# Performance work log

Measured on AMD Instinct MI355X. Metric: run time of the kernel, lower is better.

The kernel has to match this reference:

```python
import jax, jax.numpy as jnp
import numpy as np

N_SIGMA = 2
FG_W = 1.0
W_INST, W_VAR, W_SEED = 1.0, 10.0, 1.0
N_IDS = 15  # instance ids 1..15 (0 = background)


def _xym(H, W, dtype):
    # torch buffer: xm varies along width, ym along height, linspace over 512 then sliced
    xm = jnp.broadcast_to(jnp.linspace(0.0, 1.0, 512)[:W][None, :], (H, W))
    ym = jnp.broadcast_to(jnp.linspace(0.0, 1.0, 512)[:H][:, None], (H, W))
    return jnp.stack([xm, ym], 0).astype(dtype)  # [2,H,W]


def _lovasz_hinge_flat(logits, gt):
    # canonical Lovasz hinge over a flat image; gt in {0,1} float
    signs = 2.0 * gt - 1.0
    errors = 1.0 - logits * signs
    order = jnp.argsort(-errors)
    errors_sorted = errors[order]
    gt_sorted = gt[order]
    gts = gt_sorted.sum()
    inter = gts - jnp.cumsum(gt_sorted)
    union = gts + jnp.cumsum(1.0 - gt_sorted)
    jacc = 1.0 - inter / union
    grad = jnp.concatenate([jacc[:1], jacc[1:] - jacc[:-1]])
    return jnp.dot(jax.nn.relu(errors_sorted), jax.lax.stop_gradient(grad))


def _loss(prediction, instances, labels):
    B, C, H, W = prediction.shape
    xym = _xym(H, W, prediction.dtype)
    spatial_emb = jnp.tanh(prediction[:, 0:2]) + xym           # [B,2,H,W]
    sigma = prediction[:, 2:2 + N_SIGMA]                       # [B,2,H,W]
    seed = jax.nn.sigmoid(prediction[:, 2 + N_SIGMA])          # [B,H,W]

    ids = jnp.arange(1, N_IDS + 1)
    maskf = (instances[:, None] == ids[None, :, None, None]).astype(prediction.dtype)  # [B,N,H,W]
    counts = maskf.sum((-2, -1))                               # [B,N]
    valid = counts > 0
    safe = jnp.maximum(counts, 1.0)

    centers = jnp.einsum('bchw,bnhw->bnc', spatial_emb, maskf) / safe[..., None]  # [B,N,2]
    s_mean = jnp.einsum('bchw,bnhw->bnc', sigma, maskf) / safe[..., None]         # [B,N,2]
    s_sg = jax.lax.stop_gradient(s_mean)

    # sum over mask of (sigma - s_sg)^2, expanded to avoid a [B,N,2,H,W] tensor
    e2 = jnp.einsum('bchw,bnhw->bnc', sigma * sigma, maskf)
    var_sum = e2 - 2.0 * s_sg * (s_mean * safe[..., None]) + s_sg * s_sg * counts[..., None]
    var_i = var_sum.sum(-1) / (N_SIGMA * safe)                 # torch.mean over [n_sigma, M]

    s_exp = jnp.exp(10.0 * s_mean)                             # [B,N,2] (grad flows, as in torch)
    dist_arg = jnp.zeros((B, N_IDS, H, W), prediction.dtype)
    for c in range(N_SIGMA):  # tiny fixed loop over 2 coordinate channels
        d = spatial_emb[:, c][:, None] - centers[:, :, c][..., None, None]
        dist_arg = dist_arg + s_exp[:, :, c][..., None, None] * d * d
    dist = jnp.exp(-dist_arg)                                  # [B,N,H,W]

    logits = (dist * 2.0 - 1.0).reshape(B * N_IDS, H * W)
    labs = maskf.reshape(B * N_IDS, H * W)
    inst_i = jax.vmap(_lovasz_hinge_flat)(logits, labs).reshape(B, N_IDS)

    seed_i = FG_W * jnp.einsum('bnhw,bnhw->bn', maskf,
                               (seed[:, None] - jax.lax.stop_gradient(dist)) ** 2)

    bg = (labels == 0).astype(prediction.dtype)
    seed_bg = jnp.einsum('bhw,bhw->b', bg, seed * seed)        # (seed - 0)^2 on background

    vf = valid.astype(prediction.dtype)
    obj = jnp.maximum(vf.sum(1), 1.0)
    inst_b = (vf * inst_i).sum(1) / obj
    var_b = (vf * var_i).sum(1) / obj
    seed_b = (seed_bg + (vf * seed_i).sum(1)) / (H * W)
    return jnp.mean(W_INST * inst_b + W_VAR * var_b + W_SEED * seed_b)


def setup_inputs() -> dict:
    key = jax.random.key(0)
    k1, k2, k3 = jax.random.split(key, 3)
    prediction = jax.random.normal(k1, (16, 5, 512, 512), dtype=jnp.float32)
    instances = jax.random.randint(k2, (16, 512, 512), 0, 16, dtype=jnp.int64)
    labels = jax.random.randint(k3, (16, 512, 512), 0, 2, dtype=jnp.int64)
    return {"prediction": prediction, "instances": instances, "labels": labels}


def reference(prediction, instances, labels):
    return _loss(prediction, instances, labels)
```

## Files before the change

kernel.cpp:

```cpp
#include <hip/hip_runtime.h>
#include <hip/hip_fp16.h>
#include <cmath>

#define BATCH 16
#define NID   15
#define NSEG  240
#define HW    262144
#define HEADB 65536
#define NSPL  8
#define NCHK  4
#define PREBLK 512
#define PSTRIDE 112

#define KFINEBASE 30208
#define KOVF 119
#define KTOT 2424

typedef float v2f __attribute__((ext_vector_type(2)));

__device__ __forceinline__ int keyof(float d) {
  unsigned b = __float_as_uint(d);
  return (b >= 0x3B800000u) ? (int)((b >> 15) - KFINEBASE + KOVF) : (int)(b >> 23);
}
__device__ __forceinline__ void boundsof(int k, float* lo, float* hi) {
  if (k >= KOVF) {
    unsigned u = (unsigned)(k - KOVF + KFINEBASE) << 15;
    *lo = __uint_as_float(u);
    *hi = __uint_as_float(u + 32768u);
  } else {
    *lo = __uint_as_float((unsigned)k << 23);
    *hi = __uint_as_float((unsigned)(k + 1) << 23);
  }
}

__device__ __forceinline__ float fast_tanh(float x) {
  float e = __expf(2.0f * x);
  return 1.0f - 2.0f / (e + 1.0f);
}
__device__ __forceinline__ float fast_sigmoid(float x) {
  return 1.0f / (1.0f + __expf(-x));
}

struct Params { float cx, cy, e0, e1, var, valid, cnt; };
__device__ __forceinline__ Params calc_params(const float* __restrict__ st) {
  Params p;
  float cnt = st[0];
  float safe = fmaxf(cnt, 1.0f);
  p.cx = st[1] / safe;
  p.cy = st[2] / safe;
  float m0 = st[3] / safe, m1 = st[4] / safe;
  float v0 = st[5] - 2.0f * m0 * (m0 * safe) + m0 * m0 * cnt;
  float v1 = st[6] - 2.0f * m1 * (m1 * safe) + m1 * m1 * cnt;
  p.var = (v0 + v1) / (2.0f * safe);
  p.e0 = expf(10.0f * m0);
  p.e1 = expf(10.0f * m1);
  p.valid = (cnt > 0.f) ? 1.f : 0.f;
  p.cnt = cnt;
  return p;
}

__global__ void __launch_bounds__(256, 2)
pre_kernel(const float* __restrict__ pred, const int* __restrict__ inst,
           const int* __restrict__ lab, float* __restrict__ blockpart,
           unsigned* __restrict__ exyh, unsigned* __restrict__ tb8,
           unsigned* __restrict__ sd8) {
  __shared__ float ws[4][NID * 7 + 1];
  int tid = threadIdx.x;
  int w = tid >> 6, lane = tid & 63;
  int gid = blockIdx.x;
  int b = gid >> 5, c = gid & 31;
  const float* pb = pred + (size_t)b * 5 * HW;
  const int4* ip = (const int4*)(inst + (size_t)b * HW);
  const int4* lp = (const int4*)(lab + (size_t)b * HW);
  size_t bq = (size_t)b * (HW / 4);
  v2f acc[NID][4];
#pragma unroll
  for (int id = 0; id < NID; ++id)
#pragma unroll
    for (int s = 0; s < 4; ++s) acc[id][s] = (v2f)(0.f);
  float bgacc = 0.f;
  int g0 = c * 2048 + tid;
  float4 A0 = ((const float4*)pb)[g0];
  float4 A1 = ((const float4*)(pb + HW))[g0];
  float4 A2 = ((const float4*)(pb + 2 * HW))[g0];
  float4 A3 = ((const float4*)(pb + 3 * HW))[g0];
  float4 A4 = ((const float4*)(pb + 4 * HW))[g0];
  int4 T4 = ip[g0];
  int4 L4 = lp[g0];
#pragma unroll 1
  for (int it = 0; it < 8; ++it) {
    int g = c * 2048 + it * 256 + tid;
    float4 v0 = A0, v1 = A1, v2 = A2, v3 = A3, v4 = A4;
    int4 t4 = T4, l4 = L4;
    if (it < 7) {
      int gn = g + 256;
      A0 = ((const float4*)pb)[gn];
      A1 = ((const float4*)(pb + HW))[gn];
      A2 = ((const float4*)(pb + 2 * HW))[gn];
      A3 = ((const float4*)(pb + 3 * HW))[gn];
      A4 = ((const float4*)(pb + 4 * HW))[gn];
      T4 = ip[gn];
      L4 = lp[gn];
    }
    float p0a[4] = {v0.x, v0.y, v0.z, v0.w};
    float p1a[4] = {v1.x, v1.y, v1.z, v1.w};
    float p2a[4] = {v2.x, v2.y, v2.z, v2.w};
    float p3a[4] = {v3.x, v3.y, v3.z, v3.w};
    float p4a[4] = {v4.x, v4.y, v4.z, v4.w};
    int ta[4] = {t4.x, t4.y, t4.z, t4.w};
    int la[4] = {l4.x, l4.y, l4.z, l4.w};
    unsigned eo[4], tpack = 0, spack = 0;
    int px0 = g * 4;
#pragma unroll
    for (int k = 0; k < 4; ++k) {
      int px = px0 + k;
      float xm = (float)(px & 511) * (1.0f / 511.0f);
      float ym = (float)(px >> 9) * (1.0f / 511.0f);
      float ex = fast_tanh(p0a[k]) + xm;
      float ey = fast_tanh(p1a[k]) + ym;
      float sd = fast_sigmoid(p4a[k]);
      __half2 h = __floats2half2_rn(ex, ey);
      eo[k] = *reinterpret_cast<unsigned*>(&h);
      int t = ta[k];
      tpack |= ((unsigned)(t & 255)) << (8 * k);
      unsigned sq = (unsigned)(sd * 255.0f + 0.5f);
      spack |= (sq & 255u) << (8 * k);
      float p2 = p2a[k], p3 = p3a[k];
      v2f P01; P01.x = 1.0f; P01.y = ex;
      v2f P23; P23.x = ey;   P23.y = p2;
      v2f P45; P45.x = p3;   P45.y = p2 * p2;
      v2f P67; P67.x = p3 * p3; P67.y = 0.f;
#pragma unroll
      for (int id = 0; id < NID; ++id) {
        float pr = (t == id + 1) ? 1.0f : 0.0f;
        v2f prv; prv.x = pr; prv.y = pr;
        acc[id][0] = prv * P01 + acc[id][0];
        acc[id][1] = prv * P23 + acc[id][1];
        acc[id][2] = prv * P45 + acc[id][2];
        acc[id][3] = prv * P67 + acc[id][3];
      }
      if (la[k] == 0) bgacc += sd * sd;
    }
    ((uint4*)exyh)[bq + g] = make_uint4(eo[0], eo[1], eo[2], eo[3]);
    tb8[bq + g] = tpack;
    sd8[bq + g] = spack;
  }
#pragma unroll
  for (int id = 0; id < NID; ++id) {
    float vals7[7] = {acc[id][0].x, acc[id][0].y, acc[id][1].x, acc[id][1].y,
                      acc[id][2].x, acc[id][2].y, acc[id][3].x};
#pragma unroll
    for (int s = 0; s < 7; ++s) {
      float v = vals7[s];
      for (int off = 32; off > 0; off >>= 1) v += __shfl_down(v, off, 64);
      if (lane == 0) ws[w][id * 7 + s] = v;
    }
  }
  for (int off = 32; off > 0; off >>= 1) bgacc += __shfl_down(bgacc, off, 64);
  if (lane == 0) ws[w][NID * 7] = bgacc;
  __syncthreads();
  float* bp = blockpart + (size_t)gid * PSTRIDE;
  for (int i = tid; i < NID * 7 + 1; i += 256)
    bp[i] = ws[0][i] + ws[1][i] + ws[2][i] + ws[3][i];
}

__global__ void reduce_kernel(const float* __restrict__ blockpart, float* __restrict__ stats,
                              float* __restrict__ seedbg) {
  int s = blockIdx.x;
  int b = blockIdx.y;
  int tid = threadIdx.x;
  float v = (tid < 32) ? blockpart[(size_t)(b * 32 + tid) * PSTRIDE + s] : 0.f;
  for (int off = 32; off > 0; off >>= 1) v += __shfl_down(v, off, 64);
  if (tid == 0) {
    if (s < NID * 7) {
      int id = s / 7, st = s % 7;
      stats[(b * NID + id) * 8 + st] = v;
    } else {
      seedbg[b] = v;
    }
  }
}

__global__ void __launch_bounds__(512)
hist_kernel(const unsigned* __restrict__ exyh, const unsigned* __restrict__ tb8,
            const unsigned* __restrict__ sd8, const float* __restrict__ stats,
            unsigned* __restrict__ partPN, float* __restrict__ seedi) {
  int split = blockIdx.x;
  int chunk = blockIdx.y;
  int b = blockIdx.z;
  int seg0 = chunk * 4;
  __shared__ unsigned lhist[4 * KTOT];
  __shared__ float prm[4][5];
  int tid = threadIdx.x;
  if (tid < 4) {
    int gs = seg0 + tid;
    if (gs < NID) {
      Params pp = calc_params(stats + (size_t)(b * NID + gs) * 8);
      prm[tid][0] = pp.cx; prm[tid][1] = pp.cy; prm[tid][2] = pp.e0; prm[tid][3] = pp.e1;
      prm[tid][4] = pp.valid;
    } else {
      prm[tid][4] = 0.f;
    }
  }
  for (int k = tid; k < 4 * KTOT; k += 512) lhist[k] = 0u;
  __syncthreads();
  float cxr[4], cyr[4], e0r[4], e1r[4];
  bool vr[4];
#pragma unroll
  for (int n = 0; n < 4; ++n) {
    cxr[n] = prm[n][0]; cyr[n] = prm[n][1]; e0r[n] = prm[n][2]; e1r[n] = prm[n][3];
    vr[n] = (prm[n][4] != 0.f);
  }
  const uint4* ev = (const uint4*)exyh + (size_t)b * (HW / 4);
  const unsigned* tv = tb8 + (size_t)b * (HW / 4);
  const unsigned* sv = sd8 + (size_t)b * (HW / 4);
  int lane = tid & 63;
  int wid = tid >> 6;
  int swl = (lane * 21) & 63;
  float sacc[4] = {0.f, 0.f, 0.f, 0.f};
  int g = split * 8192 + wid * 64 + swl;
  uint4 ee = ev[g];
  unsigned tp = tv[g];
  unsigned sp = sv[g];
  for (int it = 0; it < 16; ++it) {
    uint4 ne; unsigned ntp, nsp;
    int ng = g + 512;
    if (it < 15) { ne = ev[ng]; ntp = tv[ng]; nsp = sv[ng]; }
    unsigned ew[4] = {ee.x, ee.y, ee.z, ee.w};
#pragma unroll
    for (int k = 0; k < 4; ++k) {
      unsigned u = ew[k];
      __half2 h = *reinterpret_cast<__half2*>(&u);
      float2 e = __half22float2(h);
      int t = (int)((tp >> (8 * k)) & 255u);
#pragma unroll
      for (int n = 0; n < 4; ++n) {
        if (!vr[n]) continue;
        float dx = e.x - cxr[n];
        float dy = e.y - cyr[n];
        float d = __expf(-(e0r[n] * dx * dx + e1r[n] * dy * dy));
        int key = keyof(d);
        bool pos = (t == seg0 + n + 1);
        atomicAdd(&lhist[n * KTOT + key], pos ? 65536u : 1u);
        if (pos) {
          float sd = (float)((sp >> (8 * k)) & 255u) * (1.0f / 255.0f);
          float df = sd - d;
          sacc[n] += df * df;
        }
      }
    }
    if (it < 15) { ee = ne; tp = ntp; sp = nsp; g = ng; }
  }
#pragma unroll
  for (int n = 0; n < 4; ++n) {
    float v = sacc[n];
    for (int off = 32; off > 0; off >>= 1) v += __shfl_down(v, off, 64);
    if (lane == 0 && v != 0.f) atomicAdd(&seedi[b * NID + seg0 + n], v);
  }
  __syncthreads();
#pragma unroll
  for (int n = 0; n < 4; ++n) {
    int gs = seg0 + n;
    if (gs >= NID) break;
    size_t base = ((size_t)(b * NID + gs) * NSPL + split) * KTOT;
    for (int k = tid; k < KTOT; k += 512) partPN[base + k] = lhist[n * KTOT + k];
  }
}

__global__ void __launch_bounds__(1024)
lovasz_kernel(const unsigned* __restrict__ partPN, const float* __restrict__ stats,
              float* __restrict__ instAcc) {
  __shared__ int histP[KTOT];
  __shared__ int histN[KTOT];
  __shared__ int PreP[KTOT + 1];
  __shared__ int PreN[KTOT + 1];
  __shared__ int wtP[16];
  __shared__ int wtN[16];
  __shared__ float wred[16];
  __shared__ float prm[2];
  int seg = blockIdx.x;
  int tid = threadIdx.x;
  int lane = tid & 63, w = tid >> 6;
  if (tid == 0) {
    Params pp = calc_params(stats + (size_t)seg * 8);
    prm[0] = pp.valid;
    prm[1] = pp.cnt;
  }
  __syncthreads();
  if (prm[0] == 0.f) {
    if (tid == 0) instAcc[seg] = 0.f;
    return;
  }
  int P = (int)prm[1];
  int Nn = HW - P;
  for (int k = tid; k < KTOT; k += 1024) {
    int sp = 0, sn = 0;
#pragma unroll
    for (int s = 0; s < NSPL; ++s) {
      unsigned v = partPN[((size_t)seg * NSPL + s) * KTOT + k];
      sp += (int)(v >> 16);
      sn += (int)(v & 0xFFFFu);
    }
    histP[k] = sp;
    histN[k] = sn;
  }
  __syncthreads();
  {
    int base = tid * 3;
    int p0 = (base < KTOT) ? histP[base] : 0;
    int p1 = (base + 1 < KTOT) ? histP[base + 1] : 0;
    int p2 = (base + 2 < KTOT) ? histP[base + 2] : 0;
    int n0 = (base < KTOT) ? histN[base] : 0;
    int n1 = (base + 1 < KTOT) ? histN[base + 1] : 0;
    int n2 = (base + 2 < KTOT) ? histN[base + 2] : 0;
    int ap = p0 + p1 + p2, an = n0 + n1 + n2;
    int sip = ap, sin_ = an;
    for (int off = 1; off < 64; off <<= 1) {
      int up = __shfl_up(sip, off, 64);
      int un = __shfl_up(sin_, off, 64);
      if (lane >= off) { sip += up; sin_ += un; }
    }
    if (lane == 63) { wtP[w] = sip; wtN[w] = sin_; }
    __syncthreads();
    int woffP = 0, woffN = 0, totP = 0, totN = 0;
#pragma unroll
    for (int j = 0; j < 16; ++j) {
      int tp = wtP[j], tn = wtN[j];
      totP += tp; totN += tn;
      if (j < w) { woffP += tp; woffN += tn; }
    }
    int exP = woffP + sip - ap;
    int exN = woffN + sin_ - an;
    if (base < KTOT) {
      PreP[base] = exP;
      PreN[base] = exN;
    }
    if (base + 1 < KTOT) {
      PreP[base + 1] = exP + p0;
      PreN[base + 1] = exN + n0;
    }
    if (base + 2 < KTOT) {
      PreP[base + 2] = exP + p0 + p1;
      PreN[base + 2] = exN + n0 + n1;
    }
    if (tid == 0) {
      PreP[KTOT] = totP;
      PreN[KTOT] = totN;
    }
    __syncthreads();
  }
  float acc = 0.f;
  for (int k = tid; k < KTOT; k += 1024) {
    int hp = histP[k], hn = histN[k];
    if ((hp | hn) == 0) continue;
    float lo, hi;
    boundsof(k, &lo, &hi);
    float m = 0.5f * (lo + hi);
    m = fminf(m, __uint_as_float(0x3F7FFFFFu));
    float tv = 1.0f - m;
    int j = keyof(tv);
    float jlo, jhi;
    boundsof(j, &jlo, &jhi);
    float den = jhi - jlo;
    float fr = (den > 0.f) ? (tv - jlo) / den : 0.5f;
    fr = fminf(fmaxf(fr, 0.f), 1.f);
    if (hp) {
      float q = (float)(Nn - PreN[j + 1]) + (1.0f - fr) * (float)histN[j];
      float a = 2.0f - 2.0f * m;
      acc += (float)hp * a / ((float)P + q);
    }
    if (hn) {
      float p = (float)PreP[j] + fr * (float)histP[j];
      int R = Nn - PreN[k + 1];
      float u0 = 1.0f / (float)(P + R);
      float u1 = 1.0f / (float)(P + R + hn);
      acc += (2.0f * m) * ((float)P - p) * (u0 - u1);
    }
  }
  for (int off = 32; off > 0; off >>= 1) acc += __shfl_down(acc, off, 64);
  if (lane == 0) wred[w] = acc;
  __syncthreads();
  if (w == 0) {
    float v = (lane < 16) ? wred[lane] : 0.f;
    for (int off = 8; off > 0; off >>= 1) v += __shfl_down(v, off, 64);
    if (lane == 0) instAcc[seg] = v;
  }
}

__global__ void final_kernel(const float* __restrict__ stats, const float* __restrict__ instAcc,
                             const float* __restrict__ seediAcc, const float* __restrict__ seedbg,
                             float* __restrict__ out) {
  int b = threadIdx.x;
  __shared__ float red[64];
  float lb = 0.f;
  if (b < BATCH) {
    float sv = 0.f, si = 0.f, svar = 0.f, ssd = 0.f;
    for (int n = 0; n < NID; ++n) {
      Params pp = calc_params(stats + (size_t)(b * NID + n) * 8);
      float vf = pp.valid;
      sv += vf;
      si += vf * instAcc[b * NID + n];
      svar += vf * pp.var;
      ssd += vf * seediAcc[b * NID + n];
    }
    float obj = fmaxf(sv, 1.0f);
    lb = si / obj + 10.0f * (svar / obj) + (seedbg[b] + ssd) / (float)HW;
  }
  red[threadIdx.x] = lb;
  __syncthreads();
  for (int s = 32; s > 0; s >>= 1) {
    if (threadIdx.x < s) red[threadIdx.x] += red[threadIdx.x + s];
    __syncthreads();
  }
  if (threadIdx.x == 0) out[0] = red[0] / (float)BATCH;
}

extern "C" void kernel_launch(void* const* d_in, const int* in_sizes, int n_in,
                              void* d_out, int out_size, void* d_ws, size_t ws_size,
                              hipStream_t stream) {
  const float* pred = (const float*)d_in[0];
  const int* inst = (const int*)d_in[1];
  const int* lab = (const int*)d_in[2];
  float* out = (float*)d_out;

  float* wsf = (float*)d_ws;
  float* seediAcc = wsf;
  float* stats = wsf + 240;
  float* instAcc = wsf + 2160;
  float* seedbg = wsf + 2400;
  char* p = (char*)d_ws + HEADB;
  unsigned* exyh = (unsigned*)p;            p += (size_t)BATCH * HW * 4;
  unsigned* tb8 = (unsigned*)p;             p += (size_t)BATCH * HW;
  unsigned* sd8 = (unsigned*)p;             p += (size_t)BATCH * HW;
  unsigned* partPN = (unsigned*)p;          p += (size_t)NSEG * NSPL * KTOT * 4;
  float* blockpart = (float*)p;

  hipMemsetAsync(seediAcc, 0, 240 * sizeof(float), stream);
  pre_kernel<<<PREBLK, 256, 0, stream>>>(pred, inst, lab, blockpart, exyh, tb8, sd8);
  reduce_kernel<<<dim3(NID * 7 + 1, BATCH), 64, 0, stream>>>(blockpart, stats, seedbg);
  hist_kernel<<<dim3(NSPL, NCHK, BATCH), 512, 0, stream>>>(exyh, tb8, sd8, stats, partPN, seediAcc);
  lovasz_kernel<<<NSEG, 1024, 0, stream>>>(partPN, stats, instAcc);
  final_kernel<<<1, 64, 0, stream>>>(stats, instAcc, seediAcc, seedbg, out);
}
```

Baseline: 252.9 us.

## Fold stats reduction into consumers, drop memset, split hist launch in two

```diff
diff --git a/kernel.cpp b/kernel.cpp
--- a/kernel.cpp
+++ b/kernel.cpp
@@ -8,7 +8,6 @@
 #define HW    262144
 #define HEADB 65536
 #define NSPL  8
-#define NCHK  4
 #define PREBLK 512
 #define PSTRIDE 112
 
@@ -59,15 +58,27 @@
   return p;
 }
 
+__device__ __forceinline__ float sum_partials(const float* __restrict__ blockpart,
+                                              int b, int slot) {
+  const float* bp = blockpart + (size_t)(b * 32) * PSTRIDE + slot;
+  float v = 0.f;
+#pragma unroll
+  for (int i = 0; i < 32; ++i) v += bp[(size_t)i * PSTRIDE];
+  return v;
+}
+
 __global__ void __launch_bounds__(256, 2)
 pre_kernel(const float* __restrict__ pred, const int* __restrict__ inst,
            const int* __restrict__ lab, float* __restrict__ blockpart,
            unsigned* __restrict__ exyh, unsigned* __restrict__ tb8,
-           unsigned* __restrict__ sd8) {
+           unsigned* __restrict__ sd8, float* __restrict__ seediAcc) {
   __shared__ float ws[4][NID * 7 + 1];
   int tid = threadIdx.x;
   int w = tid >> 6, lane = tid & 63;
   int gid = blockIdx.x;
+  if (gid == 0) {
+    for (int i = tid; i < NSEG; i += 256) seediAcc[i] = 0.f;
+  }
   int b = gid >> 5, c = gid & 31;
   const float* pb = pred + (size_t)b * 5 * HW;
   const int4* ip = (const int4*)(inst + (size_t)b * HW);
@@ -164,45 +175,37 @@
     bp[i] = ws[0][i] + ws[1][i] + ws[2][i] + ws[3][i];
 }
 
-__global__ void reduce_kernel(const float* __restrict__ blockpart, float* __restrict__ stats,
-                              float* __restrict__ seedbg) {
-  int s = blockIdx.x;
-  int b = blockIdx.y;
-  int tid = threadIdx.x;
-  float v = (tid < 32) ? blockpart[(size_t)(b * 32 + tid) * PSTRIDE + s] : 0.f;
-  for (int off = 32; off > 0; off >>= 1) v += __shfl_down(v, off, 64);
-  if (tid == 0) {
-    if (s < NID * 7) {
-      int id = s / 7, st = s % 7;
-      stats[(b * NID + id) * 8 + st] = v;
-    } else {
-      seedbg[b] = v;
-    }
-  }
-}
-
 __global__ void __launch_bounds__(512)
 hist_kernel(const unsigned* __restrict__ exyh, const unsigned* __restrict__ tb8,
-            const unsigned* __restrict__ sd8, const float* __restrict__ stats,
-            unsigned* __restrict__ partPN, float* __restrict__ seedi) {
+            const unsigned* __restrict__ sd8, const float* __restrict__ blockpart,
+            unsigned* __restrict__ partPN, float* __restrict__ seedi, int cpair) {
   int split = blockIdx.x;
-  int chunk = blockIdx.y;
+  int chunk = cpair * 2 + blockIdx.y;
   int b = blockIdx.z;
   int seg0 = chunk * 4;
   __shared__ unsigned lhist[4 * KTOT];
+  __shared__ float st8[4][8];
   __shared__ float prm[4][5];
   int tid = threadIdx.x;
+  if (tid < 28) {
+    int n = tid / 7, s = tid - n * 7;
+    int gs = seg0 + n;
+    float v = 0.f;
+    if (gs < NID) v = sum_partials(blockpart, b, gs * 7 + s);
+    st8[n][s] = v;
+  }
+  for (int k = tid; k < 4 * KTOT; k += 512) lhist[k] = 0u;
+  __syncthreads();
   if (tid < 4) {
     int gs = seg0 + tid;
     if (gs < NID) {
-      Params pp = calc_params(stats + (size_t)(b * NID + gs) * 8);
+      Params pp = calc_params(st8[tid]);
       prm[tid][0] = pp.cx; prm[tid][1] = pp.cy; prm[tid][2] = pp.e0; prm[tid][3] = pp.e1;
       prm[tid][4] = pp.valid;
     } else {
       prm[tid][4] = 0.f;
     }
   }
-  for (int k = tid; k < 4 * KTOT; k += 512) lhist[k] = 0u;
   __syncthreads();
   float cxr[4], cyr[4], e0r[4], e1r[4];
   bool vr[4];
@@ -268,8 +271,8 @@
 }
 
 __global__ void __launch_bounds__(1024)
-lovasz_kernel(const unsigned* __restrict__ partPN, const float* __restrict__ stats,
-              float* __restrict__ instAcc) {
+lovasz_kernel(const unsigned* __restrict__ partPN, const float* __restrict__ blockpart,
+              float* __restrict__ instAcc, float2* __restrict__ varv) {
   __shared__ int histP[KTOT];
   __shared__ int histN[KTOT];
   __shared__ int PreP[KTOT + 1];
@@ -277,14 +280,19 @@
   __shared__ int wtP[16];
   __shared__ int wtN[16];
   __shared__ float wred[16];
+  __shared__ float st[8];
   __shared__ float prm[2];
   int seg = blockIdx.x;
   int tid = threadIdx.x;
   int lane = tid & 63, w = tid >> 6;
+  int sb = seg / NID, sn = seg - sb * NID;
+  if (tid < 7) st[tid] = sum_partials(blockpart, sb, sn * 7 + tid);
+  __syncthreads();
   if (tid == 0) {
-    Params pp = calc_params(stats + (size_t)seg * 8);
+    Params pp = calc_params(st);
     prm[0] = pp.valid;
     prm[1] = pp.cnt;
+    varv[seg] = make_float2(pp.valid, pp.var);
   }
   __syncthreads();
   if (prm[0] == 0.f) {
@@ -294,15 +302,15 @@
   int P = (int)prm[1];
   int Nn = HW - P;
   for (int k = tid; k < KTOT; k += 1024) {
-    int sp = 0, sn = 0;
+    int sp = 0, sn2 = 0;
 #pragma unroll
     for (int s = 0; s < NSPL; ++s) {
       unsigned v = partPN[((size_t)seg * NSPL + s) * KTOT + k];
       sp += (int)(v >> 16);
-      sn += (int)(v & 0xFFFFu);
+      sn2 += (int)(v & 0xFFFFu);
     }
     histP[k] = sp;
-    histN[k] = sn;
+    histN[k] = sn2;
   }
   __syncthreads();
   {
@@ -387,24 +395,24 @@
   }
 }
 
-__global__ void final_kernel(const float* __restrict__ stats, const float* __restrict__ instAcc,
-                             const float* __restrict__ seediAcc, const float* __restrict__ seedbg,
-                             float* __restrict__ out) {
+__global__ void final_kernel(const float* __restrict__ instAcc, const float2* __restrict__ varv,
+                             const float* __restrict__ seediAcc,
+                             const float* __restrict__ blockpart, float* __restrict__ out) {
   int b = threadIdx.x;
   __shared__ float red[64];
   float lb = 0.f;
   if (b < BATCH) {
+    float seedbg = sum_partials(blockpart, b, NID * 7);
     float sv = 0.f, si = 0.f, svar = 0.f, ssd = 0.f;
     for (int n = 0; n < NID; ++n) {
-      Params pp = calc_params(stats + (size_t)(b * NID + n) * 8);
-      float vf = pp.valid;
-      sv += vf;
-      si += vf * instAcc[b * NID + n];
-      svar += vf * pp.var;
-      ssd += vf * seediAcc[b * NID + n];
+      float2 vv = varv[b * NID + n];
+      sv += vv.x;
+      si += vv.x * instAcc[b * NID + n];
+      svar += vv.x * vv.y;
+      ssd += vv.x * seediAcc[b * NID + n];
     }
     float obj = fmaxf(sv, 1.0f);
-    lb = si / obj + 10.0f * (svar / obj) + (seedbg[b] + ssd) / (float)HW;
+    lb = si / obj + 10.0f * (svar / obj) + (seedbg + ssd) / (float)HW;
   }
   red[threadIdx.x] = lb;
   __syncthreads();
@@ -425,9 +433,8 @@
 
   float* wsf = (float*)d_ws;
   float* seediAcc = wsf;
-  float* stats = wsf + 240;
+  float2* varv = (float2*)(wsf + 240);
   float* instAcc = wsf + 2160;
-  float* seedbg = wsf + 2400;
   char* p = (char*)d_ws + HEADB;
   unsigned* exyh = (unsigned*)p;            p += (size_t)BATCH * HW * 4;
   unsigned* tb8 = (unsigned*)p;             p += (size_t)BATCH * HW;
@@ -435,10 +442,9 @@
   unsigned* partPN = (unsigned*)p;          p += (size_t)NSEG * NSPL * KTOT * 4;
   float* blockpart = (float*)p;
 
-  hipMemsetAsync(seediAcc, 0, 240 * sizeof(float), stream);
-  pre_kernel<<<PREBLK, 256, 0, stream>>>(pred, inst, lab, blockpart, exyh, tb8, sd8);
-  reduce_kernel<<<dim3(NID * 7 + 1, BATCH), 64, 0, stream>>>(blockpart, stats, seedbg);
-  hist_kernel<<<dim3(NSPL, NCHK, BATCH), 512, 0, stream>>>(exyh, tb8, sd8, stats, partPN, seediAcc);
-  lovasz_kernel<<<NSEG, 1024, 0, stream>>>(partPN, stats, instAcc);
-  final_kernel<<<1, 64, 0, stream>>>(stats, instAcc, seediAcc, seedbg, out);
-}
+  pre_kernel<<<PREBLK, 256, 0, stream>>>(pred, inst, lab, blockpart, exyh, tb8, sd8, seediAcc);
+  hist_kernel<<<dim3(NSPL, 2, BATCH), 512, 0, stream>>>(exyh, tb8, sd8, blockpart, partPN, seediAcc, 0);
+  hist_kernel<<<dim3(NSPL, 2, BATCH), 512, 0, stream>>>(exyh, tb8, sd8, blockpart, partPN, seediAcc, 1);
+  lovasz_kernel<<<NSEG, 1024, 0, stream>>>(partPN, blockpart, instAcc, varv);
+  final_kernel<<<1, 64, 0, stream>>>(instAcc, varv, seediAcc, blockpart, out);
+}
```

Result: no change. 251.0 us (-0.8%).
